# Kernel tuning notes

Measured on AMD Instinct MI355X. Metric: run time of the kernel, lower is better.

Reference implementation:

```python
import jax, jax.numpy as jnp
import numpy as np

GROUP = 128  # AWQ default group size
SHIFTS = jnp.arange(8, dtype=jnp.int32) * 4  # 8 int4 nibbles per int32


def _unpack(q):
    # q: [R, C] int32 -> [R, 8*C] int4 values in [0, 15]
    return ((q[:, :, None] >> SHIFTS) & 0xF).reshape(q.shape[0], -1)


def _dequant(qweight, scales, qzeros):
    # qweight: [K, N//8] int32, scales: [K//G, N] f32, qzeros: [K//G, N//8] int32
    q = _unpack(qweight).astype(scales.dtype)            # [K, N]
    z = _unpack(qzeros).astype(scales.dtype)             # [K//G, N]
    return (q - jnp.repeat(z, GROUP, axis=0)) * jnp.repeat(scales, GROUP, axis=0)


def _pack(key, K, N):
    # pack random int4 weights into int32 words, nibble i -> column 8*j + i
    q4 = jax.random.randint(key, (K, N // 8, 8), 0, 16, dtype=jnp.int32)
    packed = jnp.zeros((K, N // 8), dtype=jnp.int32)
    for i in range(8):
        packed = packed | (q4[:, :, i] << (4 * i))
    return packed


def setup_inputs() -> dict:
    key = jax.random.key(0)
    ks = jax.random.split(key, 10)
    K, I, O = 4096, 11008, 4096  # in_features, intermediate_size, out_features
    G = GROUP
    x = jax.random.normal(ks[0], (2, 2048, K), dtype=jnp.float32)
    gate_qweight = _pack(ks[1], K, I)
    gate_qzeros = _pack(ks[2], K // G, I)
    gate_scales = jax.random.uniform(ks[3], (K // G, I), minval=1e-3, maxval=1e-2, dtype=jnp.float32)
    up_qweight = _pack(ks[4], K, I)
    up_qzeros = _pack(ks[5], K // G, I)
    up_scales = jax.random.uniform(ks[6], (K // G, I), minval=1e-3, maxval=1e-2, dtype=jnp.float32)
    down_qweight = _pack(ks[7], I, O)
    down_qzeros = _pack(ks[8], I // G, O)
    down_scales = jax.random.uniform(ks[9], (I // G, O), minval=1e-3, maxval=1e-2, dtype=jnp.float32)
    return dict(x=x,
                gate_qweight=gate_qweight, gate_scales=gate_scales, gate_qzeros=gate_qzeros,
                up_qweight=up_qweight, up_scales=up_scales, up_qzeros=up_qzeros,
                down_qweight=down_qweight, down_scales=down_scales, down_qzeros=down_qzeros)


def reference(x, gate_qweight, gate_scales, gate_qzeros,
              up_qweight, up_scales, up_qzeros,
              down_qweight, down_scales, down_qzeros):
    lead = x.shape[:-1]
    xf = x.reshape(-1, x.shape[-1])                       # [T, K]
    wg = _dequant(gate_qweight, gate_scales, gate_qzeros)  # [K, I]
    wu = _dequant(up_qweight, up_scales, up_qzeros)        # [K, I]
    wd = _dequant(down_qweight, down_scales, down_qzeros)  # [I, O]
    h = jax.nn.silu(xf @ wg) * (xf @ wu)                   # [T, I]
    out = h @ wd                                           # [T, O]
    return out.reshape(lead + (wd.shape[1],))
```

## Files before the change

### kernel.cpp

```cpp
#include <hip/hip_runtime.h>
#include <hip/hip_bf16.h>

#define T_TOK 4096
#define KDIM  4096
#define IDIM  11008
#define ODIM  4096

typedef __bf16 bf16x8 __attribute__((ext_vector_type(8)));
typedef float  f32x4  __attribute__((ext_vector_type(4)));
typedef unsigned short ushort_t;

__device__ __forceinline__ void glds16(const void* g, void* l) {
  __builtin_amdgcn_global_load_lds(
      (const __attribute__((address_space(1))) void*)g,
      (__attribute__((address_space(3))) void*)l, 16, 0, 0);
}

__global__ void k_f32_to_bf16(const float4* __restrict__ x,
                              ushort4* __restrict__ o, int n4) {
  int i = blockIdx.x * 256 + threadIdx.x;
  if (i >= n4) return;
  float4 v = x[i];
  __hip_bfloat16 b0 = __float2bfloat16(v.x);
  __hip_bfloat16 b1 = __float2bfloat16(v.y);
  __hip_bfloat16 b2 = __float2bfloat16(v.z);
  __hip_bfloat16 b3 = __float2bfloat16(v.w);
  ushort4 r;
  r.x = *(ushort_t*)&b0; r.y = *(ushort_t*)&b1;
  r.z = *(ushort_t*)&b2; r.w = *(ushort_t*)&b3;
  o[i] = r;
}

__global__ void k_dequant_t(const int* __restrict__ qw,
                            const float* __restrict__ sc,
                            const int* __restrict__ qz,
                            __hip_bfloat16* __restrict__ wt,
                            int K, int N) {
  __shared__ __align__(16) __hip_bfloat16 tile[64][72];
  const int n0 = blockIdx.x * 64;
  const int k0 = blockIdx.y * 64;
  const int t  = threadIdx.x;
  const int Nw = N >> 3;
  const int grp = k0 >> 7;
  const int jj = t & 7;
  const int zword = qz[(size_t)grp * Nw + (n0 >> 3) + jj];
  float s[8];
#pragma unroll
  for (int i = 0; i < 8; ++i) s[i] = sc[(size_t)grp * N + n0 + jj * 8 + i];
#pragma unroll
  for (int r = 0; r < 2; ++r) {
    const int kk = (t >> 3) + r * 32;
    const int word = qw[(size_t)(k0 + kk) * Nw + (n0 >> 3) + jj];
#pragma unroll
    for (int i = 0; i < 8; ++i) {
      const int q = (word >> (4 * i)) & 0xF;
      const int z = (zword >> (4 * i)) & 0xF;
      tile[jj * 8 + i][kk] = __float2bfloat16((float)(q - z) * s[i]);
    }
  }
  __syncthreads();
  const int n  = t >> 2;
  const int kc = (t & 3) * 16;
  const float4* src = (const float4*)&tile[n][kc];
  float4* dst = (float4*)(wt + (size_t)(n0 + n) * K + k0 + kc);
  dst[0] = src[0];
  dst[1] = src[1];
}

template <int EPI>
__global__ __launch_bounds__(256, 4)
void k_gemm_bt(const __hip_bfloat16* __restrict__ A,
               const __hip_bfloat16* __restrict__ B,
               void* __restrict__ Cv, int M, int N, int K) {
  __shared__ __align__(16) __hip_bfloat16 As[2][128 * 32];
  __shared__ __align__(16) __hip_bfloat16 Bs[2][128 * 32];
  const int nblk = gridDim.x;
  const int bid  = blockIdx.y * nblk + blockIdx.x;
  const int GM   = 16;
  const int band_sz = GM * nblk;
  const int band = bid / band_sz;
  const int rrem = bid - band * band_sz;
  const int nb   = rrem / GM;
  const int mb   = band * GM + (rrem - nb * GM);
  const int n0 = nb * 128;
  const int m0 = mb * 128;

  const int t = threadIdx.x;
  const int w = t >> 6;
  const int lane = t & 63;
  const int quad = lane >> 4;
  const int lm = lane & 15;
  const int wm = w >> 1;
  const int wn = w & 1;
  f32x4 acc[4][4] = {};

  const int lrow = lane >> 2;
  const int lkc  = (lane & 3) * 8;
  const __hip_bfloat16* Ag0 = A + (size_t)(m0 + w * 32 + lrow) * K + lkc;
  const __hip_bfloat16* Ag1 = Ag0 + (size_t)16 * K;
  const __hip_bfloat16* Bg0 = B + (size_t)(n0 + w * 32 + lrow) * K + lkc;
  const __hip_bfloat16* Bg1 = Bg0 + (size_t)16 * K;
  const int lo0 = (w * 32) * 32;
  const int lo1 = (w * 32 + 16) * 32;

  for (int k0 = 0; k0 < K; k0 += 64) {
    __syncthreads();
    glds16(Ag0 + k0, &As[0][lo0]);
    glds16(Ag1 + k0, &As[0][lo1]);
    glds16(Bg0 + k0, &Bs[0][lo0]);
    glds16(Bg1 + k0, &Bs[0][lo1]);
    glds16(Ag0 + k0 + 32, &As[1][lo0]);
    glds16(Ag1 + k0 + 32, &As[1][lo1]);
    glds16(Bg0 + k0 + 32, &Bs[1][lo0]);
    glds16(Bg1 + k0 + 32, &Bs[1][lo1]);
    __syncthreads();
#pragma unroll
    for (int h = 0; h < 2; ++h) {
      bf16x8 af[4], bfr[4];
#pragma unroll
      for (int mi = 0; mi < 4; ++mi)
        af[mi] = *(const bf16x8*)&As[h][(wm * 64 + mi * 16 + lm) * 32 + quad * 8];
#pragma unroll
      for (int ni = 0; ni < 4; ++ni)
        bfr[ni] = *(const bf16x8*)&Bs[h][(wn * 64 + ni * 16 + lm) * 32 + quad * 8];
#pragma unroll
      for (int mi = 0; mi < 4; ++mi)
#pragma unroll
        for (int ni = 0; ni < 4; ++ni)
          acc[mi][ni] = __builtin_amdgcn_mfma_f32_16x16x32_bf16(
              af[mi], bfr[ni], acc[mi][ni], 0, 0, 0);
    }
  }

#pragma unroll
  for (int mi = 0; mi < 4; ++mi)
#pragma unroll
    for (int ni = 0; ni < 4; ++ni)
#pragma unroll
      for (int r = 0; r < 4; ++r) {
        const int row = m0 + wm * 64 + mi * 16 + quad * 4 + r;
        const int col = n0 + wn * 64 + ni * 16 + lm;
        const float v = acc[mi][ni][r];
        if (EPI == 0) {
          ((__hip_bfloat16*)Cv)[(size_t)row * N + col] = __float2bfloat16(v);
        } else if (EPI == 1) {
          __hip_bfloat16* H = (__hip_bfloat16*)Cv;
          const float u = __bfloat162float(H[(size_t)row * N + col]);
          const float sg = v / (1.0f + __expf(-v));
          H[(size_t)row * N + col] = __float2bfloat16(sg * u);
        } else {
          ((float*)Cv)[(size_t)row * N + col] = v;
        }
      }
}

extern "C" void kernel_launch(void* const* d_in, const int* in_sizes, int n_in,
                              void* d_out, int out_size, void* d_ws, size_t ws_size,
                              hipStream_t stream) {
  const float* x   = (const float*)d_in[0];
  const int*   gqw = (const int*)d_in[1];
  const float* gsc = (const float*)d_in[2];
  const int*   gqz = (const int*)d_in[3];
  const int*   uqw = (const int*)d_in[4];
  const float* usc = (const float*)d_in[5];
  const int*   uqz = (const int*)d_in[6];
  const int*   dqw = (const int*)d_in[7];
  const float* dsc = (const float*)d_in[8];
  const int*   dqz = (const int*)d_in[9];
  float* out = (float*)d_out;

  char* ws = (char*)d_ws;
  __hip_bfloat16* xb   = (__hip_bfloat16*)ws;
  __hip_bfloat16* wbuf = (__hip_bfloat16*)(ws + 33554432);
  __hip_bfloat16* h    = (__hip_bfloat16*)(ws + 33554432 + 90177536);

  k_f32_to_bf16<<<16384, 256, 0, stream>>>((const float4*)x, (ushort4*)xb,
                                           (T_TOK * KDIM) / 4);

  dim3 dqg(IDIM / 64, KDIM / 64);
  dim3 dqd(ODIM / 64, IDIM / 64);
  dim3 g1(IDIM / 128, T_TOK / 128);
  dim3 g2(ODIM / 128, T_TOK / 128);

  k_dequant_t<<<dqg, 256, 0, stream>>>(uqw, usc, uqz, wbuf, KDIM, IDIM);
  k_gemm_bt<0><<<g1, 256, 0, stream>>>(xb, wbuf, (void*)h, T_TOK, IDIM, KDIM);
  k_dequant_t<<<dqg, 256, 0, stream>>>(gqw, gsc, gqz, wbuf, KDIM, IDIM);
  k_gemm_bt<1><<<g1, 256, 0, stream>>>(xb, wbuf, (void*)h, T_TOK, IDIM, KDIM);
  k_dequant_t<<<dqd, 256, 0, stream>>>(dqw, dsc, dqz, wbuf, IDIM, ODIM);
  k_gemm_bt<2><<<g2, 256, 0, stream>>>(h, wbuf, (void*)out, T_TOK, ODIM, IDIM);
}
```

Measured before the change: 1.564 ms.

## Repack int4 weights to fp8 and dequantize with scales inside fp16 GEMM

The weight prepass now writes (q - z) as fp8 bytes in the transposed layout instead of scaled bf16, which halves the intermediate weight traffic. The GEMM loads fp8 weights through registers, prefetching one step ahead, then converts and scales them into fp16 in LDS before running fp16 MFMA. Activations and the intermediate h move from bf16 to fp16. This adds per-iteration conversion ALU work and a register-path B load in place of direct global-to-LDS loads, and lowers the occupancy hint from 4 to 3. fp16 also has a narrower range than bf16 for h.

After: 1.454 ms. -7.0%, faster.

```diff
diff --git a/kernel.cpp b/kernel.cpp
--- a/kernel.cpp
+++ b/kernel.cpp
@@ -1,14 +1,16 @@
 #include <hip/hip_runtime.h>
 #include <hip/hip_bf16.h>
+#include <hip/hip_fp16.h>
 
 #define T_TOK 4096
 #define KDIM  4096
 #define IDIM  11008
 #define ODIM  4096
 
-typedef __bf16 bf16x8 __attribute__((ext_vector_type(8)));
-typedef float  f32x4  __attribute__((ext_vector_type(4)));
-typedef unsigned short ushort_t;
+typedef _Float16 f16x8 __attribute__((ext_vector_type(8)));
+typedef __fp16   h16x2 __attribute__((ext_vector_type(2)));
+typedef float    f32x4 __attribute__((ext_vector_type(4)));
+typedef float    f32x2 __attribute__((ext_vector_type(2)));
 
 __device__ __forceinline__ void glds16(const void* g, void* l) {
   __builtin_amdgcn_global_load_lds(
@@ -16,27 +18,24 @@
       (__attribute__((address_space(3))) void*)l, 16, 0, 0);
 }
 
-__global__ void k_f32_to_bf16(const float4* __restrict__ x,
-                              ushort4* __restrict__ o, int n4) {
+__global__ void k_f32_to_f16(const float4* __restrict__ x,
+                             ushort4* __restrict__ o, int n4) {
   int i = blockIdx.x * 256 + threadIdx.x;
   if (i >= n4) return;
   float4 v = x[i];
-  __hip_bfloat16 b0 = __float2bfloat16(v.x);
-  __hip_bfloat16 b1 = __float2bfloat16(v.y);
-  __hip_bfloat16 b2 = __float2bfloat16(v.z);
-  __hip_bfloat16 b3 = __float2bfloat16(v.w);
+  __half h0 = __float2half(v.x), h1 = __float2half(v.y);
+  __half h2v = __float2half(v.z), h3 = __float2half(v.w);
   ushort4 r;
-  r.x = *(ushort_t*)&b0; r.y = *(ushort_t*)&b1;
-  r.z = *(ushort_t*)&b2; r.w = *(ushort_t*)&b3;
+  r.x = *(unsigned short*)&h0; r.y = *(unsigned short*)&h1;
+  r.z = *(unsigned short*)&h2v; r.w = *(unsigned short*)&h3;
   o[i] = r;
 }
 
-__global__ void k_dequant_t(const int* __restrict__ qw,
-                            const float* __restrict__ sc,
-                            const int* __restrict__ qz,
-                            __hip_bfloat16* __restrict__ wt,
-                            int K, int N) {
-  __shared__ __align__(16) __hip_bfloat16 tile[64][72];
+__global__ void k_repack_fp8(const int* __restrict__ qw,
+                             const int* __restrict__ qz,
+                             unsigned char* __restrict__ bq,
+                             int K, int N) {
+  __shared__ __align__(16) unsigned char tile[64][80];
   const int n0 = blockIdx.x * 64;
   const int k0 = blockIdx.y * 64;
   const int t  = threadIdx.x;
@@ -44,36 +43,48 @@
   const int grp = k0 >> 7;
   const int jj = t & 7;
   const int zword = qz[(size_t)grp * Nw + (n0 >> 3) + jj];
-  float s[8];
-#pragma unroll
-  for (int i = 0; i < 8; ++i) s[i] = sc[(size_t)grp * N + n0 + jj * 8 + i];
 #pragma unroll
   for (int r = 0; r < 2; ++r) {
     const int kk = (t >> 3) + r * 32;
     const int word = qw[(size_t)(k0 + kk) * Nw + (n0 >> 3) + jj];
 #pragma unroll
-    for (int i = 0; i < 8; ++i) {
-      const int q = (word >> (4 * i)) & 0xF;
-      const int z = (zword >> (4 * i)) & 0xF;
-      tile[jj * 8 + i][kk] = __float2bfloat16((float)(q - z) * s[i]);
+    for (int i = 0; i < 8; i += 2) {
+      const float v0 = (float)(((word >> (4 * i)) & 0xF) - ((zword >> (4 * i)) & 0xF));
+      const float v1 = (float)(((word >> (4 * i + 4)) & 0xF) - ((zword >> (4 * i + 4)) & 0xF));
+      const int p = __builtin_amdgcn_cvt_pk_fp8_f32(v0, v1, 0, false);
+      tile[jj * 8 + i][kk]     = (unsigned char)(p & 0xFF);
+      tile[jj * 8 + i + 1][kk] = (unsigned char)((p >> 8) & 0xFF);
     }
   }
   __syncthreads();
   const int n  = t >> 2;
   const int kc = (t & 3) * 16;
-  const float4* src = (const float4*)&tile[n][kc];
-  float4* dst = (float4*)(wt + (size_t)(n0 + n) * K + k0 + kc);
-  dst[0] = src[0];
-  dst[1] = src[1];
+  int4 v = *(const int4*)&tile[n][kc];
+  *(int4*)(bq + (size_t)(n0 + n) * K + k0 + kc) = v;
+}
+
+__device__ __forceinline__ void dq16(uint4 w, float s, __half* dst) {
+  h16x2 r[8];
+  const unsigned int ws[4] = {w.x, w.y, w.z, w.w};
+#pragma unroll
+  for (int d = 0; d < 4; ++d) {
+    f32x2 lo = __builtin_amdgcn_cvt_pk_f32_fp8((int)ws[d], false);
+    f32x2 hi = __builtin_amdgcn_cvt_pk_f32_fp8((int)ws[d], true);
+    r[d * 2]     = __builtin_amdgcn_cvt_pkrtz(lo.x * s, lo.y * s);
+    r[d * 2 + 1] = __builtin_amdgcn_cvt_pkrtz(hi.x * s, hi.y * s);
+  }
+  *(uint4*)dst       = *(const uint4*)&r[0];
+  *(uint4*)(dst + 8) = *(const uint4*)&r[4];
 }
 
 template <int EPI>
-__global__ __launch_bounds__(256, 4)
-void k_gemm_bt(const __hip_bfloat16* __restrict__ A,
-               const __hip_bfloat16* __restrict__ B,
-               void* __restrict__ Cv, int M, int N, int K) {
-  __shared__ __align__(16) __hip_bfloat16 As[2][128 * 32];
-  __shared__ __align__(16) __hip_bfloat16 Bs[2][128 * 32];
+__global__ __launch_bounds__(256, 3)
+void k_gemm_q(const __half* __restrict__ A,
+              const unsigned char* __restrict__ Bq,
+              const float* __restrict__ sc,
+              void* __restrict__ Cv, int M, int N, int K) {
+  __shared__ __align__(16) __half As[2][128 * 32];
+  __shared__ __align__(16) __half Bs[2][128 * 40];
   const int nblk = gridDim.x;
   const int bid  = blockIdx.y * nblk + blockIdx.x;
   const int GM   = 16;
@@ -96,38 +107,48 @@
 
   const int lrow = lane >> 2;
   const int lkc  = (lane & 3) * 8;
-  const __hip_bfloat16* Ag0 = A + (size_t)(m0 + w * 32 + lrow) * K + lkc;
-  const __hip_bfloat16* Ag1 = Ag0 + (size_t)16 * K;
-  const __hip_bfloat16* Bg0 = B + (size_t)(n0 + w * 32 + lrow) * K + lkc;
-  const __hip_bfloat16* Bg1 = Bg0 + (size_t)16 * K;
+  const __half* Ag0 = A + (size_t)(m0 + w * 32 + lrow) * K + lkc;
+  const __half* Ag1 = Ag0 + (size_t)16 * K;
   const int lo0 = (w * 32) * 32;
   const int lo1 = (w * 32 + 16) * 32;
 
+  const int brow = t >> 1;
+  const int bhalf = t & 1;
+  const unsigned char* bg = Bq + (size_t)(n0 + brow) * K + bhalf * 16;
+  __half* bdst0 = &Bs[0][brow * 40 + bhalf * 16];
+  __half* bdst1 = &Bs[1][brow * 40 + bhalf * 16];
+
+  float s = 0.0f;
+  uint4 bc0 = *(const uint4*)(bg);
+  uint4 bc1 = *(const uint4*)(bg + 32);
+
   for (int k0 = 0; k0 < K; k0 += 64) {
+    if ((k0 & 127) == 0) s = sc[(size_t)(k0 >> 7) * N + n0 + brow];
     __syncthreads();
     glds16(Ag0 + k0, &As[0][lo0]);
     glds16(Ag1 + k0, &As[0][lo1]);
-    glds16(Bg0 + k0, &Bs[0][lo0]);
-    glds16(Bg1 + k0, &Bs[0][lo1]);
     glds16(Ag0 + k0 + 32, &As[1][lo0]);
     glds16(Ag1 + k0 + 32, &As[1][lo1]);
-    glds16(Bg0 + k0 + 32, &Bs[1][lo0]);
-    glds16(Bg1 + k0 + 32, &Bs[1][lo1]);
+    dq16(bc0, s, bdst0);
+    dq16(bc1, s, bdst1);
     __syncthreads();
+    const int kn = (k0 + 64 < K) ? (k0 + 64) : 0;
+    bc0 = *(const uint4*)(bg + kn);
+    bc1 = *(const uint4*)(bg + kn + 32);
 #pragma unroll
     for (int h = 0; h < 2; ++h) {
-      bf16x8 af[4], bfr[4];
+      f16x8 af[4], bfr[4];
 #pragma unroll
       for (int mi = 0; mi < 4; ++mi)
-        af[mi] = *(const bf16x8*)&As[h][(wm * 64 + mi * 16 + lm) * 32 + quad * 8];
+        af[mi] = *(const f16x8*)&As[h][(wm * 64 + mi * 16 + lm) * 32 + quad * 8];
 #pragma unroll
       for (int ni = 0; ni < 4; ++ni)
-        bfr[ni] = *(const bf16x8*)&Bs[h][(wn * 64 + ni * 16 + lm) * 32 + quad * 8];
+        bfr[ni] = *(const f16x8*)&Bs[h][(wn * 64 + ni * 16 + lm) * 40 + quad * 8];
 #pragma unroll
       for (int mi = 0; mi < 4; ++mi)
 #pragma unroll
         for (int ni = 0; ni < 4; ++ni)
-          acc[mi][ni] = __builtin_amdgcn_mfma_f32_16x16x32_bf16(
+          acc[mi][ni] = __builtin_amdgcn_mfma_f32_16x16x32_f16(
               af[mi], bfr[ni], acc[mi][ni], 0, 0, 0);
     }
   }
@@ -142,12 +163,12 @@
         const int col = n0 + wn * 64 + ni * 16 + lm;
         const float v = acc[mi][ni][r];
         if (EPI == 0) {
-          ((__hip_bfloat16*)Cv)[(size_t)row * N + col] = __float2bfloat16(v);
+          ((__half*)Cv)[(size_t)row * N + col] = __float2half(v);
         } else if (EPI == 1) {
-          __hip_bfloat16* H = (__hip_bfloat16*)Cv;
-          const float u = __bfloat162float(H[(size_t)row * N + col]);
+          __half* H = (__half*)Cv;
+          const float u = __half2float(H[(size_t)row * N + col]);
           const float sg = v / (1.0f + __expf(-v));
-          H[(size_t)row * N + col] = __float2bfloat16(sg * u);
+          H[(size_t)row * N + col] = __float2half(sg * u);
         } else {
           ((float*)Cv)[(size_t)row * N + col] = v;
         }
@@ -170,22 +191,22 @@
   float* out = (float*)d_out;
 
   char* ws = (char*)d_ws;
-  __hip_bfloat16* xb   = (__hip_bfloat16*)ws;
-  __hip_bfloat16* wbuf = (__hip_bfloat16*)(ws + 33554432);
-  __hip_bfloat16* h    = (__hip_bfloat16*)(ws + 33554432 + 90177536);
-
-  k_f32_to_bf16<<<16384, 256, 0, stream>>>((const float4*)x, (ushort4*)xb,
-                                           (T_TOK * KDIM) / 4);
-
-  dim3 dqg(IDIM / 64, KDIM / 64);
-  dim3 dqd(ODIM / 64, IDIM / 64);
+  __half*        xb = (__half*)ws;
+  unsigned char* bq = (unsigned char*)(ws + 33554432);
+  __half*        h  = (__half*)(ws + 33554432 + 45088768);
+
+  k_f32_to_f16<<<16384, 256, 0, stream>>>((const float4*)x, (ushort4*)xb,
+                                          (T_TOK * KDIM) / 4);
+
+  dim3 rpg(IDIM / 64, KDIM / 64);
+  dim3 rpd(ODIM / 64, IDIM / 64);
   dim3 g1(IDIM / 128, T_TOK / 128);
   dim3 g2(ODIM / 128, T_TOK / 128);
 
-  k_dequant_t<<<dqg, 256, 0, stream>>>(uqw, usc, uqz, wbuf, KDIM, IDIM);
-  k_gemm_bt<0><<<g1, 256, 0, stream>>>(xb, wbuf, (void*)h, T_TOK, IDIM, KDIM);
-  k_dequant_t<<<dqg, 256, 0, stream>>>(gqw, gsc, gqz, wbuf, KDIM, IDIM);
-  k_gemm_bt<1><<<g1, 256, 0, stream>>>(xb, wbuf, (void*)h, T_TOK, IDIM, KDIM);
-  k_dequant_t<<<dqd, 256, 0, stream>>>(dqw, dsc, dqz, wbuf, IDIM, ODIM);
-  k_gemm_bt<2><<<g2, 256, 0, stream>>>(h, wbuf, (void*)out, T_TOK, ODIM, IDIM);
-}
+  k_repack_fp8<<<rpg, 256, 0, stream>>>(uqw, uqz, bq, KDIM, IDIM);
+  k_gemm_q<0><<<g1, 256, 0, stream>>>(xb, bq, usc, (void*)h, T_TOK, IDIM, KDIM);
+  k_repack_fp8<<<rpg, 256, 0, stream>>>(gqw, gqz, bq, KDIM, IDIM);
+  k_gemm_q<1><<<g1, 256, 0, stream>>>(xb, bq, gsc, (void*)h, T_TOK, IDIM, KDIM);
+  k_repack_fp8<<<rpd, 256, 0, stream>>>(dqw, dqz, bq, IDIM, ODIM);
+  k_gemm_q<2><<<g2, 256, 0, stream>>>(h, bq, dsc, (void*)out, T_TOK, ODIM, IDIM);
+}
```
